# Performance work log

Measured on AMD Instinct MI355X. Metric: run time of the kernel, lower is better.

Reference implementation:

```python
import jax, jax.numpy as jnp
import numpy as np

B, A, H = 128, 24, 256
N, E = B * A, B * A * A
MAX_ATOMS, TIME_DIM, TEXT_DIM, NFREQ, NLAYERS = 103, 256, 128, 10, 4
DIS_DIM = NFREQ * 2 * 3  # 60
EDGE_IN = 2 * H + 9 + DIS_DIM  # 581


def setup_inputs() -> dict:
    key = jax.random.key(0)
    ks = iter(jax.random.split(key, 40))
    def nrm(shape, fan_in):
        return jax.random.normal(next(ks), shape, jnp.float32) / np.sqrt(fan_in).astype(np.float32)
    # fully-connected block-diagonal edges per graph (incl. self-loops), as dense_to_sparse(block_diag(ones))
    ii = jnp.repeat(jnp.arange(A, dtype=jnp.int32), A)
    jj = jnp.tile(jnp.arange(A, dtype=jnp.int32), A)
    off = (jnp.arange(B, dtype=jnp.int32) * A)[:, None]
    edges = jnp.stack([(off + ii[None, :]).reshape(-1), (off + jj[None, :]).reshape(-1)])  # [2,E]
    node2graph = jnp.repeat(jnp.arange(B, dtype=jnp.int32), A)  # [N]
    edge2graph = node2graph[edges[0]]  # [E]
    return dict(
        atom_types=jax.random.normal(next(ks), (N, MAX_ATOMS), jnp.float32),
        frac_coords=jax.random.uniform(next(ks), (N, 3), jnp.float32),
        lattices=jax.random.normal(next(ks), (B, 3, 3), jnp.float32),
        t=jax.random.normal(next(ks), (B, TIME_DIM), jnp.float32),
        text_embeds=jax.random.normal(next(ks), (B, TEXT_DIM), jnp.float32),
        w_emb=nrm((H, MAX_ATOMS), MAX_ATOMS), b_emb=jnp.zeros((H,), jnp.float32),
        w_cond=nrm((2 * H, TIME_DIM + TEXT_DIM), TIME_DIM + TEXT_DIM), b_cond=jnp.zeros((2 * H,), jnp.float32),
        w_proj=nrm((H, H), H), b_proj=jnp.zeros((H,), jnp.float32),
        film_g=jnp.ones((H,), jnp.float32), film_b=jnp.zeros((H,), jnp.float32),
        edge_w1=nrm((NLAYERS, H, EDGE_IN), EDGE_IN), edge_b1=jnp.zeros((NLAYERS, H), jnp.float32),
        edge_w2=nrm((NLAYERS, H, H), H), edge_b2=jnp.zeros((NLAYERS, H), jnp.float32),
        node_w1=nrm((NLAYERS, H, 2 * H), 2 * H), node_b1=jnp.zeros((NLAYERS, H), jnp.float32),
        node_w2=nrm((NLAYERS, H, H), H), node_b2=jnp.zeros((NLAYERS, H), jnp.float32),
        w_coord=nrm((3, H), H), w_latt=nrm((9, H), H),
        w_type=nrm((MAX_ATOMS, H), H), b_type=jnp.zeros((MAX_ATOMS,), jnp.float32),
        edges=edges, node2graph=node2graph, edge2graph=edge2graph,
    )


def _layernorm(x, g, b):
    mu = jnp.mean(x, -1, keepdims=True)
    v = jnp.mean((x - mu) ** 2, -1, keepdims=True)
    return (x - mu) * jax.lax.rsqrt(v + 1e-5) * g + b


def reference(atom_types, frac_coords, lattices, t, text_embeds,
              w_emb, b_emb, w_cond, b_cond, w_proj, b_proj, film_g, film_b,
              edge_w1, edge_b1, edge_w2, edge_b2, node_w1, node_b1, node_w2, node_b2,
              w_coord, w_latt, w_type, b_type, edges, node2graph, edge2graph):
    silu = jax.nn.silu
    e0, e1 = edges[0], edges[1]
    # gen_edges (fc): periodic fractional difference per edge
    frac_diff = (frac_coords[e1] - frac_coords[e0]) % 1.0  # [E,3]
    # SinusoidsEmbedding (detached in the original)
    freqs = 2.0 * jnp.pi * jnp.arange(NFREQ, dtype=jnp.float32)
    emb = (frac_diff[..., None] * freqs).reshape(frac_diff.shape[0], 3 * NFREQ)
    demb = jax.lax.stop_gradient(jnp.concatenate([jnp.sin(emb), jnp.cos(emb)], -1))  # [E,60]
    # lattice inner products (ip=True), gathered per edge
    lat_ips = jnp.einsum('bij,bkj->bik', lattices, lattices).reshape(-1, 9)
    lat_e = lat_ips[edge2graph]  # [E,9]
    # FiLM conditioning (identical every layer) -- repeat_interleave per atom == gather by node2graph
    cond = silu(jnp.concatenate([t, text_embeds], -1) @ w_cond.T + b_cond)[node2graph]  # [N,2H]
    scale, shift = cond[:, :H], cond[:, H:]
    deg = jnp.maximum(jax.ops.segment_sum(jnp.ones((e0.shape[0],), jnp.float32), e0, num_segments=N), 1.0)
    nf = atom_types @ w_emb.T + b_emb  # smooth node embedding: Linear(max_atoms, H)
    for i in range(NLAYERS):
        # FiLM layer
        y = _layernorm(nf @ w_proj.T + b_proj, film_g, film_b)
        nf = nf + silu(y * scale + shift)
        # CSPLayer edge model: gather -> concat -> 2-layer MLP
        ein = jnp.concatenate([nf[e0], nf[e1], lat_e, demb], -1)  # [E, 581]
        ef = silu(ein @ edge_w1[i].T + edge_b1[i])
        ef = silu(ef @ edge_w2[i].T + edge_b2[i])
        # node model: scatter_mean over source nodes, then 2-layer MLP, residual
        agg = jax.ops.segment_sum(ef, e0, num_segments=N) / deg[:, None]
        no = silu(jnp.concatenate([nf, agg], -1) @ node_w1[i].T + node_b1[i])
        no = silu(no @ node_w2[i].T + node_b2[i])
        nf = nf + no
    coords_out = nf @ w_coord.T  # [N,3]
    gfeat = jax.ops.segment_sum(nf, node2graph, num_segments=B) / jnp.float32(A)  # scatter mean over graphs
    lattice_out = (gfeat @ w_latt.T).reshape(-1, 3, 3)
    lattice_out = jnp.einsum('bij,bjk->bik', lattice_out, lattices)  # ip=True
    atom_types_out = nf @ w_type.T + b_type  # [N,103]
    return atom_types_out, lattice_out, coords_out, nf
```

## Files before the change

### kernel.cpp

```cpp
#include <hip/hip_runtime.h>
#include <math.h>

#define B_      128
#define A_      24
#define N_      3072
#define NLAYERS 4

#define OFF_COND    0
#define OFF_LATW    65536
#define OFF_NFMIDH  196608
#define OFF_AGGH    589824
#define OFF_PARTIH  983040
#define OFF_PARTJH  1376256
#define OFF_W1LATT  1769472
#define OFF_PW1A    1778688
#define OFF_PW1B    1909760
#define OFF_PW1D    2040832
#define OFF_PW2     2073600
#define OFF_PWPROJ  2204672
#define OFF_PNW1    2237440
#define OFF_PNW2    2499584
#define OFF_PWEMB   2630656
#define OFF_PWCOND  2647040
#define OFF_PWTYPE  2745344

#define OUT_TYPES  0
#define OUT_LATT   316416
#define OUT_COORD  317568
#define OUT_NF     326784

typedef __attribute__((ext_vector_type(8))) short bf16x8;
typedef __attribute__((ext_vector_type(4))) float f32x4;

__device__ __forceinline__ float silu_f(float x) { return x / (1.0f + __expf(-x)); }
__device__ __forceinline__ unsigned short f2bf(float x) {
    unsigned int u = __float_as_uint(x);
    return (unsigned short)((u + 0x7FFFu + ((u >> 16) & 1u)) >> 16);
}
__device__ __forceinline__ float bf2f(unsigned short h) {
    return __uint_as_float(((unsigned int)h) << 16);
}

__global__ void k_prep(const float* w_emb, const float* w_cond, const float* w_proj,
                       const float* ew1, const float* ew2, const float* nw1, const float* nw2,
                       const float* w_type, float* ws) {
    int idx = blockIdx.x * blockDim.x + threadIdx.x;
    unsigned short* pu = (unsigned short*)ws;
    int i = idx;
    if (i < 9216)   { int l = i / 2304, r = (i % 2304) / 256, h = i % 256;
                      ws[OFF_W1LATT + i] = ew1[((size_t)l * 256 + h) * 581 + 512 + r]; return; }        i -= 9216;
    if (i < 262144) { int l = i >> 16, r = i & 65535, ks = r >> 13, r2 = r & 8191,
                      nt = r2 >> 9, r3 = r2 & 511, lane = r3 >> 3, j = r3 & 7;
                      int k = ks * 32 + (lane >> 4) * 8 + j, n = nt * 16 + (lane & 15);
                      pu[(size_t)OFF_PW1A * 2 + i] = f2bf(ew1[((size_t)l * 256 + n) * 581 + k]); return; } i -= 262144;
    if (i < 262144) { int l = i >> 16, r = i & 65535, ks = r >> 13, r2 = r & 8191,
                      nt = r2 >> 9, r3 = r2 & 511, lane = r3 >> 3, j = r3 & 7;
                      int k = ks * 32 + (lane >> 4) * 8 + j, n = nt * 16 + (lane & 15);
                      pu[(size_t)OFF_PW1B * 2 + i] = f2bf(ew1[((size_t)l * 256 + n) * 581 + 256 + k]); return; } i -= 262144;
    if (i < 65536)  { int l = i >> 14, r = i & 16383, ks = r >> 13, r2 = r & 8191,
                      nt = r2 >> 9, r3 = r2 & 511, lane = r3 >> 3, j = r3 & 7;
                      int kp = ks * 32 + (lane >> 4) * 8 + j, n = nt * 16 + (lane & 15);
                      float v = (kp < 60) ? ew1[((size_t)l * 256 + n) * 581 + 521 + kp] : 0.0f;
                      pu[(size_t)OFF_PW1D * 2 + i] = f2bf(v); return; }                                  i -= 65536;
    if (i < 262144) { int l = i >> 16, r = i & 65535, ks = r >> 13, r2 = r & 8191,
                      nt = r2 >> 9, r3 = r2 & 511, lane = r3 >> 3, j = r3 & 7;
                      int k = ks * 32 + (lane >> 4) * 8 + j, n = nt * 16 + (lane & 15);
                      pu[(size_t)OFF_PW2 * 2 + i] = f2bf(ew2[((size_t)l * 256 + n) * 256 + k]); return; } i -= 262144;
    if (i < 65536)  { int ks = i >> 13, r2 = i & 8191,
                      nt = r2 >> 9, r3 = r2 & 511, lane = r3 >> 3, j = r3 & 7;
                      int k = ks * 32 + (lane >> 4) * 8 + j, n = nt * 16 + (lane & 15);
                      pu[(size_t)OFF_PWPROJ * 2 + i] = f2bf(w_proj[(size_t)n * 256 + k]); return; }      i -= 65536;
    if (i < 524288) { int l = i >> 17, r = i & 131071, ks = r >> 13, r2 = r & 8191,
                      nt = r2 >> 9, r3 = r2 & 511, lane = r3 >> 3, j = r3 & 7;
                      int k = ks * 32 + (lane >> 4) * 8 + j, n = nt * 16 + (lane & 15);
                      pu[(size_t)OFF_PNW1 * 2 + i] = f2bf(nw1[((size_t)l * 256 + n) * 512 + k]); return; } i -= 524288;
    if (i < 262144) { int l = i >> 16, r = i & 65535, ks = r >> 13, r2 = r & 8191,
                      nt = r2 >> 9, r3 = r2 & 511, lane = r3 >> 3, j = r3 & 7;
                      int k = ks * 32 + (lane >> 4) * 8 + j, n = nt * 16 + (lane & 15);
                      pu[(size_t)OFF_PNW2 * 2 + i] = f2bf(nw2[((size_t)l * 256 + n) * 256 + k]); return; } i -= 262144;
    if (i < 32768)  { int ks = i >> 13, r2 = i & 8191,
                      nt = r2 >> 9, r3 = r2 & 511, lane = r3 >> 3, j = r3 & 7;
                      int k = ks * 32 + (lane >> 4) * 8 + j, n = nt * 16 + (lane & 15);
                      float v = (k < 103) ? w_emb[(size_t)n * 103 + k] : 0.0f;
                      pu[(size_t)OFF_PWEMB * 2 + i] = f2bf(v); return; }                                 i -= 32768;
    if (i < 196608) { int ks = i / 16384, r2 = i & 16383,
                      nt = r2 >> 9, r3 = r2 & 511, lane = r3 >> 3, j = r3 & 7;
                      int k = ks * 32 + (lane >> 4) * 8 + j, n = nt * 16 + (lane & 15);
                      pu[(size_t)OFF_PWCOND * 2 + i] = f2bf(w_cond[(size_t)n * 384 + k]); return; }      i -= 196608;
    { int ks = i / 3584, r2 = i % 3584,
      nt = r2 >> 9, r3 = r2 & 511, lane = r3 >> 3, j = r3 & 7;
      int k = ks * 32 + (lane >> 4) * 8 + j, a = nt * 16 + (lane & 15);
      float v = (a < 103) ? w_type[(size_t)a * 256 + k] : 0.0f;
      pu[(size_t)OFF_PWTYPE * 2 + i] = f2bf(v); }
}

__global__ void __launch_bounds__(256) k_setup(const float* lat, const float* t_in, const float* tx,
                                               const float* b_cond, float* ws) {
    __shared__ __align__(16) unsigned short s_ct[16][392];
    __shared__ float s_lat[16][9];
    int tid = threadIdx.x, w = tid >> 6, ln = tid & 63;
    int l15 = ln & 15, g = ln >> 4;
    int g0 = blockIdx.x * 16;
    if (tid < 144) {
        int gl = tid / 9, r = tid % 9, ii = r / 3, kk = r % 3;
        const float* L = lat + (g0 + gl) * 9;
        s_lat[gl][r] = L[ii*3+0]*L[kk*3+0] + L[ii*3+1]*L[kk*3+1] + L[ii*3+2]*L[kk*3+2];
    }
    for (int idx = tid; idx < 16 * 384; idx += 256) {
        int row = idx / 384, k = idx % 384;
        float v = (k < 256) ? t_in[(size_t)(g0 + row) * 256 + k] : tx[(size_t)(g0 + row) * 128 + (k - 256)];
        s_ct[row][k] = f2bf(v);
    }
    __syncthreads();
    for (int idx = tid; idx < 16384; idx += 256) {
        int l = idx >> 12, gl = (idx >> 8) & 15, h = idx & 255;
        float a = 0.f;
#pragma unroll
        for (int r = 0; r < 9; r++) a += s_lat[gl][r] * ws[OFF_W1LATT + (l * 9 + r) * 256 + h];
        ws[OFF_LATW + (size_t)(l * 128 + g0 + gl) * 256 + h] = a;
    }
    const unsigned short* pc = (const unsigned short*)ws + (size_t)OFF_PWCOND * 2;
    f32x4 acc[8] = {};
    for (int ks = 0; ks < 12; ks++) {
        bf16x8 a = *(const bf16x8*)&s_ct[l15][ks * 32 + g * 8];
#pragma unroll
        for (int q = 0; q < 8; q++) {
            int nt = w * 8 + q;
            bf16x8 bf = *(const bf16x8*)&pc[((size_t)(ks * 32 + nt) * 64 + ln) * 8];
            acc[q] = __builtin_amdgcn_mfma_f32_16x16x32_bf16(a, bf, acc[q], 0, 0, 0);
        }
    }
#pragma unroll
    for (int q = 0; q < 8; q++) {
        int col = w * 128 + q * 16 + l15;
        float bc = b_cond[col];
#pragma unroll
        for (int r = 0; r < 4; r++) {
            int gg = g0 + 4 * g + r;
            ws[OFF_COND + (size_t)gg * 512 + col] = silu_f(acc[q][r] + bc);
        }
    }
}

__global__ void __launch_bounds__(512) k_fnf(int l, const float* at, const float* b_emb,
                                             const float* nb1, const float* nb2,
                                             const float* b_proj, const float* film_g, const float* film_b,
                                             const float* eb1, float* ws) {
    __shared__ __align__(16) unsigned short s_in[16][536];
    __shared__ __align__(16) unsigned short s_h[16][264];
    __shared__ __align__(16) unsigned short s_a[16][264];
    __shared__ float s_nf[16][260];
    __shared__ float s_mu[16], s_rs[16];
    float (*s_c)[268] = (float(*)[268])&s_in[0][0];
    int tid = threadIdx.x, w = tid >> 6, ln = tid & 63;
    int l15 = ln & 15, g = ln >> 4;
    int n0 = blockIdx.x * 16;
    const unsigned short* wsu = (const unsigned short*)ws;
    unsigned short* wsw = (unsigned short*)ws;

    f32x4 accn[2] = {};
    if (l == 0) {
        for (int idx = tid; idx < 16 * 128; idx += 512) {
            int row = idx >> 7, k = idx & 127;
            s_in[row][k] = (k < 103) ? f2bf(at[(size_t)(n0 + row) * 103 + k]) : (unsigned short)0;
        }
        __syncthreads();
        const unsigned short* pe = wsu + (size_t)OFF_PWEMB * 2;
        for (int ks = 0; ks < 4; ks++) {
            bf16x8 a = *(const bf16x8*)&s_in[l15][ks * 32 + g * 8];
#pragma unroll
            for (int q = 0; q < 2; q++) {
                bf16x8 bf = *(const bf16x8*)&pe[((size_t)(ks * 16 + 2 * w + q) * 64 + ln) * 8];
                accn[q] = __builtin_amdgcn_mfma_f32_16x16x32_bf16(a, bf, accn[q], 0, 0, 0);
            }
        }
        __syncthreads();
#pragma unroll
        for (int q = 0; q < 2; q++) {
            int col = w * 32 + q * 16 + l15;
            float be = b_emb[col];
#pragma unroll
            for (int r = 0; r < 4; r++) {
                int row = 4 * g + r;
                float v = accn[q][r] + be;
                s_nf[row][col] = v;
                s_a[row][col] = f2bf(v);
            }
        }
    } else {
        int lp = l - 1;
        const unsigned short* nfmidh = wsu + (size_t)OFF_NFMIDH * 2;
        const unsigned short* aggh   = wsu + (size_t)OFF_AGGH * 2;
        {
            int row = tid >> 5, c8 = tid & 31;
            *(uint4*)&s_in[row][c8 * 8]       = *(const uint4*)&nfmidh[(size_t)(n0 + row) * 256 + c8 * 8];
            *(uint4*)&s_in[row][256 + c8 * 8] = *(const uint4*)&aggh[(size_t)(n0 + row) * 256 + c8 * 8];
        }
        __syncthreads();
        const unsigned short* p1 = wsu + (size_t)OFF_PNW1 * 2 + (size_t)lp * 131072;
        f32x4 acc[2] = {};
        for (int ks = 0; ks < 16; ks++) {
            bf16x8 a = *(const bf16x8*)&s_in[l15][ks * 32 + g * 8];
#pragma unroll
            for (int q = 0; q < 2; q++) {
                bf16x8 bf = *(const bf16x8*)&p1[((size_t)(ks * 16 + 2 * w + q) * 64 + ln) * 8];
                acc[q] = __builtin_amdgcn_mfma_f32_16x16x32_bf16(a, bf, acc[q], 0, 0, 0);
            }
        }
#pragma unroll
        for (int q = 0; q < 2; q++) {
            int col = w * 32 + q * 16 + l15;
            float b1 = nb1[lp * 256 + col];
#pragma unroll
            for (int r = 0; r < 4; r++) s_h[4 * g + r][col] = f2bf(silu_f(acc[q][r] + b1));
        }
        __syncthreads();
        const unsigned short* p2 = wsu + (size_t)OFF_PNW2 * 2 + (size_t)lp * 65536;
        for (int ks = 0; ks < 8; ks++) {
            bf16x8 a = *(const bf16x8*)&s_h[l15][ks * 32 + g * 8];
#pragma unroll
            for (int q = 0; q < 2; q++) {
                bf16x8 bf = *(const bf16x8*)&p2[((size_t)(ks * 16 + 2 * w + q) * 64 + ln) * 8];
                accn[q] = __builtin_amdgcn_mfma_f32_16x16x32_bf16(a, bf, accn[q], 0, 0, 0);
            }
        }
#pragma unroll
        for (int q = 0; q < 2; q++) {
            int col = w * 32 + q * 16 + l15;
            float b2 = nb2[lp * 256 + col];
#pragma unroll
            for (int r = 0; r < 4; r++) {
                int row = 4 * g + r;
                float v = bf2f(s_in[row][col]) + silu_f(accn[q][r] + b2);
                s_nf[row][col] = v;
                s_a[row][col] = f2bf(v);
            }
        }
    }
    __syncthreads();
    const unsigned short* pwp = wsu + (size_t)OFF_PWPROJ * 2;
    f32x4 accp[2] = {};
    for (int ks = 0; ks < 8; ks++) {
        bf16x8 a = *(const bf16x8*)&s_a[l15][ks * 32 + g * 8];
#pragma unroll
        for (int q = 0; q < 2; q++) {
            bf16x8 bf = *(const bf16x8*)&pwp[((size_t)(ks * 16 + 2 * w + q) * 64 + ln) * 8];
            accp[q] = __builtin_amdgcn_mfma_f32_16x16x32_bf16(a, bf, accp[q], 0, 0, 0);
        }
    }
    __syncthreads();
#pragma unroll
    for (int q = 0; q < 2; q++) {
        int col = w * 32 + q * 16 + l15;
        float bp = b_proj[col];
#pragma unroll
        for (int r = 0; r < 4; r++) s_c[4 * g + r][col] = accp[q][r] + bp;
    }
    __syncthreads();
    for (int r2 = 0; r2 < 2; r2++) {
        int row = w * 2 + r2;
        float s = 0.f, q = 0.f;
        for (int c = ln; c < 256; c += 64) { float v = s_c[row][c]; s += v; q += v * v; }
#pragma unroll
        for (int o = 1; o < 64; o <<= 1) { s += __shfl_xor(s, o); q += __shfl_xor(q, o); }
        if (ln == 0) {
            float mu = s * (1.0f / 256.0f);
            float var = q * (1.0f / 256.0f) - mu * mu;
            s_mu[row] = mu; s_rs[row] = rsqrtf(var + 1e-5f);
        }
    }
    __syncthreads();
    {
        int col = tid & 255, rb = tid >> 8;
        float gg = film_g[col], bb = film_b[col];
        unsigned short* nfmidh = wsw + (size_t)OFF_NFMIDH * 2;
#pragma unroll
        for (int t = 0; t < 8; t++) {
            int row = rb + 2 * t;
            int n = n0 + row, b = n / 24;
            float sc = ws[OFF_COND + (size_t)b * 512 + col];
            float sh = ws[OFF_COND + (size_t)b * 512 + 256 + col];
            float yn = (s_c[row][col] - s_mu[row]) * s_rs[row] * gg + bb;
            float outv = s_nf[row][col] + silu_f(yn * sc + sh);
            unsigned short ob = f2bf(outv);
            nfmidh[(size_t)n * 256 + col] = ob;
            s_a[row][col] = ob;
        }
    }
    __syncthreads();
    const unsigned short* pA = wsu + (size_t)OFF_PW1A * 2 + (size_t)l * 65536;
    const unsigned short* pB = wsu + (size_t)OFF_PW1B * 2 + (size_t)l * 65536;
    f32x4 aI[2] = {}, aJ[2] = {};
    for (int ks = 0; ks < 8; ks++) {
        bf16x8 a = *(const bf16x8*)&s_a[l15][ks * 32 + g * 8];
#pragma unroll
        for (int q = 0; q < 2; q++) {
            bf16x8 bi = *(const bf16x8*)&pA[((size_t)(ks * 16 + 2 * w + q) * 64 + ln) * 8];
            bf16x8 bj = *(const bf16x8*)&pB[((size_t)(ks * 16 + 2 * w + q) * 64 + ln) * 8];
            aI[q] = __builtin_amdgcn_mfma_f32_16x16x32_bf16(a, bi, aI[q], 0, 0, 0);
            aJ[q] = __builtin_amdgcn_mfma_f32_16x16x32_bf16(a, bj, aJ[q], 0, 0, 0);
        }
    }
    unsigned short* partih = wsw + (size_t)OFF_PARTIH * 2;
    unsigned short* partjh = wsw + (size_t)OFF_PARTJH * 2;
#pragma unroll
    for (int q = 0; q < 2; q++) {
        int col = w * 32 + q * 16 + l15;
        float e1 = eb1[l * 256 + col];
#pragma unroll
        for (int r = 0; r < 4; r++) {
            int n = n0 + 4 * g + r;
            int gb = n / 24;
            float vi = aI[q][r] + e1 + ws[OFF_LATW + (size_t)(l * 128 + gb) * 256 + col];
            partih[(size_t)n * 256 + col] = f2bf(vi);
            partjh[(size_t)n * 256 + col] = f2bf(aJ[q][r]);
        }
    }
}

__global__ void __launch_bounds__(256, 4) k_edge(int l, const float* frac, const float* eb2, float* ws) {
    __shared__ __align__(16) unsigned short s_u[48 * 256];
    __shared__ __align__(16) unsigned short s_pJ[24][264];
    __shared__ __align__(16) unsigned short s_pI[2][264];
    __shared__ float s_fc[24][3];
    int tid = threadIdx.x, w = tid >> 6, ln = tid & 63;
    int l15 = ln & 15, g = ln >> 4;
    int b = blockIdx.x & 127, c = blockIdx.x >> 7;
    int i0 = c * 2;

    const unsigned short* partjh = (const unsigned short*)ws + (size_t)OFF_PARTJH * 2 + (size_t)b * 24 * 256;
    const unsigned short* partih = (const unsigned short*)ws + (size_t)OFF_PARTIH * 2 + (size_t)(b * 24 + i0) * 256;
    for (int idx = tid; idx < 72; idx += 256) s_fc[idx / 3][idx % 3] = frac[b * 72 + idx];
    for (int idx = tid; idx < 768; idx += 256) {
        int row = idx >> 5, c8 = idx & 31;
        *(uint4*)&s_pJ[row][c8 * 8] = *(const uint4*)&partjh[row * 256 + c8 * 8];
    }
    if (tid < 64) {
        int row = tid >> 5, c8 = tid & 31;
        *(uint4*)&s_pI[row][c8 * 8] = *(const uint4*)&partih[row * 256 + c8 * 8];
    }
    __syncthreads();
    for (int idx = tid; idx < 3072; idx += 256) {
        int row = idx >> 6, k = idx & 63;
        unsigned short v = 0;
        if (k < 60) {
            int kk = (k < 30) ? k : k - 30;
            int d = kk / 10, f = kk % 10;
            int hi = (row >= 24);
            int j = row - (hi ? 24 : 0);
            float fd = s_fc[j][d] - s_fc[i0 + hi][d];
            fd -= floorf(fd);
            float ang = fd * (6.283185307179586f * (float)f);
            v = f2bf((k < 30) ? __sinf(ang) : __cosf(ang));
        }
        s_u[(row << 6) + (((k >> 3) ^ (row & 7)) << 3) + (k & 7)] = v;
    }
    __syncthreads();

    const unsigned short* wsu = (const unsigned short*)ws;
    const unsigned short* pw1d = wsu + (size_t)OFF_PW1D * 2 + (size_t)l * 16384;
    f32x4 acc[3][4] = {};
    for (int ks = 0; ks < 2; ks++) {
        bf16x8 a[3];
        int kb = ks * 4 + g;
#pragma unroll
        for (int mt = 0; mt < 3; mt++) {
            int row = mt * 16 + l15;
            a[mt] = *(const bf16x8*)&s_u[(row << 6) + ((kb ^ (row & 7)) << 3)];
        }
#pragma unroll
        for (int nt = 0; nt < 4; nt++) {
            bf16x8 bf = *(const bf16x8*)&pw1d[((size_t)(ks * 16 + w * 4 + nt) * 64 + ln) * 8];
#pragma unroll
            for (int mt = 0; mt < 3; mt++)
                acc[mt][nt] = __builtin_amdgcn_mfma_f32_16x16x32_bf16(a[mt], bf, acc[mt][nt], 0, 0, 0);
        }
    }
    __syncthreads();
    float pIv[2][4];
#pragma unroll
    for (int hi = 0; hi < 2; hi++)
#pragma unroll
        for (int nt = 0; nt < 4; nt++) pIv[hi][nt] = bf2f(s_pI[hi][w * 64 + nt * 16 + l15]);
#pragma unroll
    for (int mt = 0; mt < 3; mt++)
#pragma unroll
        for (int nt = 0; nt < 4; nt++) {
            int col = w * 64 + nt * 16 + l15;
#pragma unroll
            for (int r = 0; r < 4; r++) {
                int row = mt * 16 + 4 * g + r;
                int hi = (row >= 24);
                int j = row - 24 * hi;
                float v = acc[mt][nt][r] + pIv[hi][nt] + bf2f(s_pJ[j][col]);
                s_u[(row << 8) + ((((col >> 3) ^ (row & 7))) << 3) + (col & 7)] = f2bf(silu_f(v));
            }
        }
    __syncthreads();
    const unsigned short* pw2 = wsu + (size_t)OFF_PW2 * 2 + (size_t)l * 65536;
    f32x4 acc2[3][4] = {};
    for (int ks = 0; ks < 8; ks++) {
        bf16x8 a[3];
        int kb = ks * 4 + g;
#pragma unroll
        for (int mt = 0; mt < 3; mt++) {
            int row = mt * 16 + l15;
            a[mt] = *(const bf16x8*)&s_u[(row << 8) + ((kb ^ (row & 7)) << 3)];
        }
#pragma unroll
        for (int nt = 0; nt < 4; nt++) {
            bf16x8 bf = *(const bf16x8*)&pw2[((size_t)(ks * 16 + w * 4 + nt) * 64 + ln) * 8];
#pragma unroll
            for (int mt = 0; mt < 3; mt++)
                acc2[mt][nt] = __builtin_amdgcn_mfma_f32_16x16x32_bf16(a[mt], bf, acc2[mt][nt], 0, 0, 0);
        }
    }
    float s0[4] = {}, s1[4] = {};
#pragma unroll
    for (int nt = 0; nt < 4; nt++) {
        int col = w * 64 + nt * 16 + l15;
        float b2 = eb2[l * 256 + col];
#pragma unroll
        for (int r = 0; r < 4; r++) s0[nt] += silu_f(acc2[0][nt][r] + b2);
        float m = 0.f;
#pragma unroll
        for (int r = 0; r < 4; r++) m += silu_f(acc2[1][nt][r] + b2);
        if (g < 2) s0[nt] += m; else s1[nt] += m;
#pragma unroll
        for (int r = 0; r < 4; r++) s1[nt] += silu_f(acc2[2][nt][r] + b2);
    }
#pragma unroll
    for (int nt = 0; nt < 4; nt++) {
        s0[nt] += __shfl_xor(s0[nt], 16);
        s0[nt] += __shfl_xor(s0[nt], 32);
        s1[nt] += __shfl_xor(s1[nt], 16);
        s1[nt] += __shfl_xor(s1[nt], 32);
    }
    unsigned short* aggh = (unsigned short*)ws + (size_t)OFF_AGGH * 2;
    if (g == 0) {
#pragma unroll
        for (int nt = 0; nt < 4; nt++) {
            int col = w * 64 + nt * 16 + l15;
            aggh[(size_t)(b * 24 + i0) * 256 + col]     = f2bf(s0[nt] * (1.0f / 24.0f));
            aggh[(size_t)(b * 24 + i0 + 1) * 256 + col] = f2bf(s1[nt] * (1.0f / 24.0f));
        }
    }
}

__global__ void __launch_bounds__(512) k_tail(const float* nb1, const float* nb2,
                                              const float* b_type, const float* w_coord,
                                              const float* lattices, const float* w_latt,
                                              float* ws, float* out) {
    __shared__ __align__(16) unsigned short s_in[32][536];
    __shared__ __align__(16) unsigned short s_h[32][264];
    __shared__ float gf[256];
    __shared__ float lo[9];
    float (*s_nf)[260] = (float(*)[260])&s_in[0][0];
    unsigned short (*s_a)[264] = s_h;
    int tid = threadIdx.x, w = tid >> 6, ln = tid & 63;
    int l15 = ln & 15, g = ln >> 4;
    int b = blockIdx.x, n0 = b * 24;
    const unsigned short* wsu = (const unsigned short*)ws;
    const int lp = 3;
    const unsigned short* nfmidh = wsu + (size_t)OFF_NFMIDH * 2;
    const unsigned short* aggh   = wsu + (size_t)OFF_AGGH * 2;
    for (int idx = tid; idx < 1024; idx += 512) {
        int row = idx >> 5, c8 = idx & 31;
        int rr = (row < 24) ? row : 0;
        *(uint4*)&s_in[row][c8 * 8]       = *(const uint4*)&nfmidh[(size_t)(n0 + rr) * 256 + c8 * 8];
        *(uint4*)&s_in[row][256 + c8 * 8] = *(const uint4*)&aggh[(size_t)(n0 + rr) * 256 + c8 * 8];
    }
    __syncthreads();
    const unsigned short* p1 = wsu + (size_t)OFF_PNW1 * 2 + (size_t)lp * 131072;
    f32x4 acc[2][2] = {};
    for (int ks = 0; ks < 16; ks++) {
        bf16x8 a0 = *(const bf16x8*)&s_in[l15][ks * 32 + g * 8];
        bf16x8 a1 = *(const bf16x8*)&s_in[16 + l15][ks * 32 + g * 8];
#pragma unroll
        for (int q = 0; q < 2; q++) {
            bf16x8 bf = *(const bf16x8*)&p1[((size_t)(ks * 16 + 2 * w + q) * 64 + ln) * 8];
            acc[0][q] = __builtin_amdgcn_mfma_f32_16x16x32_bf16(a0, bf, acc[0][q], 0, 0, 0);
            acc[1][q] = __builtin_amdgcn_mfma_f32_16x16x32_bf16(a1, bf, acc[1][q], 0, 0, 0);
        }
    }
#pragma unroll
    for (int q = 0; q < 2; q++) {
        int col = w * 32 + q * 16 + l15;
        float b1 = nb1[lp * 256 + col];
#pragma unroll
        for (int mt = 0; mt < 2; mt++)
#pragma unroll
            for (int r = 0; r < 4; r++) s_h[mt * 16 + 4 * g + r][col] = f2bf(silu_f(acc[mt][q][r] + b1));
    }
    __syncthreads();
    const unsigned short* p2 = wsu + (size_t)OFF_PNW2 * 2 + (size_t)lp * 65536;
    f32x4 a2[2][2] = {};
    for (int ks = 0; ks < 8; ks++) {
        bf16x8 a0 = *(const bf16x8*)&s_h[l15][ks * 32 + g * 8];
        bf16x8 a1 = *(const bf16x8*)&s_h[16 + l15][ks * 32 + g * 8];
#pragma unroll
        for (int q = 0; q < 2; q++) {
            bf16x8 bf = *(const bf16x8*)&p2[((size_t)(ks * 16 + 2 * w + q) * 64 + ln) * 8];
            a2[0][q] = __builtin_amdgcn_mfma_f32_16x16x32_bf16(a0, bf, a2[0][q], 0, 0, 0);
            a2[1][q] = __builtin_amdgcn_mfma_f32_16x16x32_bf16(a1, bf, a2[1][q], 0, 0, 0);
        }
    }
    float res[2][2][4];
#pragma unroll
    for (int q = 0; q < 2; q++) {
        int col = w * 32 + q * 16 + l15;
#pragma unroll
        for (int mt = 0; mt < 2; mt++)
#pragma unroll
            for (int r = 0; r < 4; r++) res[mt][q][r] = bf2f(s_in[mt * 16 + 4 * g + r][col]);
    }
    __syncthreads();
#pragma unroll
    for (int q = 0; q < 2; q++) {
        int col = w * 32 + q * 16 + l15;
        float b2 = nb2[lp * 256 + col];
#pragma unroll
        for (int mt = 0; mt < 2; mt++)
#pragma unroll
            for (int r = 0; r < 4; r++) {
                int row = mt * 16 + 4 * g + r;
                float v = res[mt][q][r] + silu_f(a2[mt][q][r] + b2);
                if (row < 24) {
                    s_nf[row][col] = v;
                    out[OUT_NF + (size_t)(n0 + row) * 256 + col] = v;
                }
                s_a[row][col] = f2bf(v);
            }
    }
    __syncthreads();
    if (w < 7) {
        const unsigned short* pt = wsu + (size_t)OFF_PWTYPE * 2;
        f32x4 at2[2] = {};
        for (int ks = 0; ks < 8; ks++) {
            bf16x8 a0 = *(const bf16x8*)&s_a[l15][ks * 32 + g * 8];
            bf16x8 a1 = *(const bf16x8*)&s_a[16 + l15][ks * 32 + g * 8];
            bf16x8 bf = *(const bf16x8*)&pt[((size_t)(ks * 7 + w) * 64 + ln) * 8];
            at2[0] = __builtin_amdgcn_mfma_f32_16x16x32_bf16(a0, bf, at2[0], 0, 0, 0);
            at2[1] = __builtin_amdgcn_mfma_f32_16x16x32_bf16(a1, bf, at2[1], 0, 0, 0);
        }
        int a_col = w * 16 + l15;
        if (a_col < 103) {
            float bt = b_type[a_col];
#pragma unroll
            for (int mt = 0; mt < 2; mt++)
#pragma unroll
                for (int r = 0; r < 4; r++) {
                    int row = mt * 16 + 4 * g + r;
                    if (row < 24)
                        out[OUT_TYPES + (size_t)(n0 + row) * 103 + a_col] = at2[mt][r] + bt;
                }
        }
    }
    if (tid < 72) {
        int p = tid / 3, cc = tid % 3;
        float a0 = 0.f;
        for (int k = 0; k < 256; k++) a0 += s_nf[p][k] * w_coord[cc * 256 + k];
        out[OUT_COORD + (size_t)(n0 + p) * 3 + cc] = a0;
    }
    if (tid < 256) {
        float s = 0.f;
#pragma unroll
        for (int i = 0; i < 24; i++) s += s_nf[i][tid];
        gf[tid] = s * (1.0f / 24.0f);
    }
    __syncthreads();
    if (tid < 9) {
        float a0 = 0.f;
        for (int k = 0; k < 256; k++) a0 += gf[k] * w_latt[tid * 256 + k];
        lo[tid] = a0;
    }
    __syncthreads();
    if (tid < 9) {
        int i = tid / 3, kk = tid % 3;
        float a0 = 0.f;
#pragma unroll
        for (int j = 0; j < 3; j++) a0 += lo[i * 3 + j] * lattices[b * 9 + j * 3 + kk];
        out[OUT_LATT + (size_t)b * 9 + tid] = a0;
    }
}

extern "C" void kernel_launch(void* const* d_in, const int* in_sizes, int n_in,
                              void* d_out, int out_size, void* d_ws, size_t ws_size,
                              hipStream_t stream) {
    const float* atom_types = (const float*)d_in[0];
    const float* frac       = (const float*)d_in[1];
    const float* lattices   = (const float*)d_in[2];
    const float* t_in       = (const float*)d_in[3];
    const float* text       = (const float*)d_in[4];
    const float* w_emb      = (const float*)d_in[5];
    const float* b_emb      = (const float*)d_in[6];
    const float* w_cond     = (const float*)d_in[7];
    const float* b_cond     = (const float*)d_in[8];
    const float* w_proj     = (const float*)d_in[9];
    const float* b_proj     = (const float*)d_in[10];
    const float* film_g     = (const float*)d_in[11];
    const float* film_b     = (const float*)d_in[12];
    const float* ew1        = (const float*)d_in[13];
    const float* eb1        = (const float*)d_in[14];
    const float* ew2        = (const float*)d_in[15];
    const float* eb2        = (const float*)d_in[16];
    const float* nw1        = (const float*)d_in[17];
    const float* nb1        = (const float*)d_in[18];
    const float* nw2        = (const float*)d_in[19];
    const float* nb2        = (const float*)d_in[20];
    const float* w_coord    = (const float*)d_in[21];
    const float* w_latt     = (const float*)d_in[22];
    const float* w_type     = (const float*)d_in[23];
    const float* b_type     = (const float*)d_in[24];
    float* ws  = (float*)d_ws;
    float* out = (float*)d_out;

    k_prep<<<7700, 256, 0, stream>>>(w_emb, w_cond, w_proj, ew1, ew2, nw1, nw2, w_type, ws);
    k_setup<<<8, 256, 0, stream>>>(lattices, t_in, text, b_cond, ws);
    for (int l = 0; l < NLAYERS; l++) {
        k_fnf<<<N_ / 16, 512, 0, stream>>>(l, atom_types, b_emb, nb1, nb2,
                                           b_proj, film_g, film_b, eb1, ws);
        k_edge<<<N_ * 12 / 24, 256, 0, stream>>>(l, frac, eb2, ws);
    }
    k_tail<<<B_, 512, 0, stream>>>(nb1, nb2, b_type, w_coord, lattices, w_latt, ws, out);
}
```

Measured before the change: 348.8 us.

## Precompute distance embeddings once and fold node partials into edge MFMA via one-hot

The sinusoidal distance embedding for every edge tile is now computed once in the prep kernel and stored in bf16 in the workspace. Each edge layer loads it instead of recomputing sin/cos. The per-node I and J partial sums are also added through an extra MFMA K-step, using one-hot selector columns in the A tile and the partial rows as the B operand, which removes the shared-memory staging and per-element adds in the epilogue. The cost is a much larger prep launch that writes about 9 MB of embeddings, global reads of that buffer in each of the 4 layers, and one extra MFMA step per tile. The one-hot path also adds the partials in bf16 precision inside the MFMA.

```diff
diff --git a/kernel.cpp b/kernel.cpp
--- a/kernel.cpp
+++ b/kernel.cpp
@@ -23,6 +23,7 @@
 #define OFF_PWEMB   2630656
 #define OFF_PWCOND  2647040
 #define OFF_PWTYPE  2745344
+#define OFF_DEMBG   2759680
 
 #define OUT_TYPES  0
 #define OUT_LATT   316416
@@ -43,7 +44,7 @@
 
 __global__ void k_prep(const float* w_emb, const float* w_cond, const float* w_proj,
                        const float* ew1, const float* ew2, const float* nw1, const float* nw2,
-                       const float* w_type, float* ws) {
+                       const float* w_type, const float* frac, float* ws) {
     int idx = blockIdx.x * blockDim.x + threadIdx.x;
     unsigned short* pu = (unsigned short*)ws;
     int i = idx;
@@ -87,11 +88,27 @@
                       nt = r2 >> 9, r3 = r2 & 511, lane = r3 >> 3, j = r3 & 7;
                       int k = ks * 32 + (lane >> 4) * 8 + j, n = nt * 16 + (lane & 15);
                       pu[(size_t)OFF_PWCOND * 2 + i] = f2bf(w_cond[(size_t)n * 384 + k]); return; }      i -= 196608;
-    { int ks = i / 3584, r2 = i % 3584,
-      nt = r2 >> 9, r3 = r2 & 511, lane = r3 >> 3, j = r3 & 7;
-      int k = ks * 32 + (lane >> 4) * 8 + j, a = nt * 16 + (lane & 15);
-      float v = (a < 103) ? w_type[(size_t)a * 256 + k] : 0.0f;
-      pu[(size_t)OFF_PWTYPE * 2 + i] = f2bf(v); }
+    if (i < 28672)  { int ks = i / 3584, r2 = i % 3584,
+                      nt = r2 >> 9, r3 = r2 & 511, lane = r3 >> 3, j = r3 & 7;
+                      int k = ks * 32 + (lane >> 4) * 8 + j, a = nt * 16 + (lane & 15);
+                      float v = (a < 103) ? w_type[(size_t)a * 256 + k] : 0.0f;
+                      pu[(size_t)OFF_PWTYPE * 2 + i] = f2bf(v); return; }                                i -= 28672;
+    if (i < 4718592) {
+        int u = i / 3072, r2 = i % 3072, row = r2 >> 6, k = r2 & 63;
+        int bb = u / 12, c = u % 12, i0 = 2 * c;
+        unsigned short v = 0;
+        if (k < 60) {
+            int kk = (k < 30) ? k : k - 30;
+            int d = kk / 10, f = kk % 10;
+            int hi = (row >= 24);
+            int j = row - 24 * hi;
+            float fd = frac[(bb * 24 + j) * 3 + d] - frac[(bb * 24 + i0 + hi) * 3 + d];
+            fd -= floorf(fd);
+            float ang = fd * (6.283185307179586f * (float)f);
+            v = f2bf((k < 30) ? __sinf(ang) : __cosf(ang));
+        }
+        pu[(size_t)OFF_DEMBG * 2 + i] = v;
+    }
 }
 
 __global__ void __launch_bounds__(256) k_setup(const float* lat, const float* t_in, const float* tx,
@@ -318,70 +335,68 @@
     }
 }
 
-__global__ void __launch_bounds__(256, 4) k_edge(int l, const float* frac, const float* eb2, float* ws) {
+__global__ void __launch_bounds__(256, 4) k_edge(int l, const float* eb2, float* ws) {
     __shared__ __align__(16) unsigned short s_u[48 * 256];
-    __shared__ __align__(16) unsigned short s_pJ[24][264];
-    __shared__ __align__(16) unsigned short s_pI[2][264];
-    __shared__ float s_fc[24][3];
     int tid = threadIdx.x, w = tid >> 6, ln = tid & 63;
     int l15 = ln & 15, g = ln >> 4;
     int b = blockIdx.x & 127, c = blockIdx.x >> 7;
-    int i0 = c * 2;
-
-    const unsigned short* partjh = (const unsigned short*)ws + (size_t)OFF_PARTJH * 2 + (size_t)b * 24 * 256;
-    const unsigned short* partih = (const unsigned short*)ws + (size_t)OFF_PARTIH * 2 + (size_t)(b * 24 + i0) * 256;
-    for (int idx = tid; idx < 72; idx += 256) s_fc[idx / 3][idx % 3] = frac[b * 72 + idx];
-    for (int idx = tid; idx < 768; idx += 256) {
-        int row = idx >> 5, c8 = idx & 31;
-        *(uint4*)&s_pJ[row][c8 * 8] = *(const uint4*)&partjh[row * 256 + c8 * 8];
-    }
-    if (tid < 64) {
-        int row = tid >> 5, c8 = tid & 31;
-        *(uint4*)&s_pI[row][c8 * 8] = *(const uint4*)&partih[row * 256 + c8 * 8];
-    }
-    __syncthreads();
-    for (int idx = tid; idx < 3072; idx += 256) {
-        int row = idx >> 6, k = idx & 63;
-        unsigned short v = 0;
-        if (k < 60) {
-            int kk = (k < 30) ? k : k - 30;
-            int d = kk / 10, f = kk % 10;
-            int hi = (row >= 24);
-            int j = row - (hi ? 24 : 0);
-            float fd = s_fc[j][d] - s_fc[i0 + hi][d];
-            fd -= floorf(fd);
-            float ang = fd * (6.283185307179586f * (float)f);
-            v = f2bf((k < 30) ? __sinf(ang) : __cosf(ang));
-        }
-        s_u[(row << 6) + (((k >> 3) ^ (row & 7)) << 3) + (k & 7)] = v;
-    }
-    __syncthreads();
-
+    int i0 = c * 2, n0i = b * 24;
     const unsigned short* wsu = (const unsigned short*)ws;
+
+    const unsigned short* partih = wsu + (size_t)OFF_PARTIH * 2;
+    const unsigned short* partjh = wsu + (size_t)OFF_PARTJH * 2;
+    bf16x8 bp[4];
+#pragma unroll
+    for (int nt = 0; nt < 4; nt++) {
+        int col = w * 64 + nt * 16 + l15;
+#pragma unroll
+        for (int e = 0; e < 8; e++) {
+            int kp = g * 8 + e;
+            unsigned short v = 0;
+            if (kp < 2)       v = partih[(size_t)(n0i + i0 + kp) * 256 + col];
+            else if (kp < 26) v = partjh[(size_t)(n0i + kp - 2) * 256 + col];
+            bp[nt][e] = (short)v;
+        }
+    }
+    const unsigned short* dg = wsu + (size_t)OFF_DEMBG * 2 + (size_t)(b * 12 + c) * 3072;
+    for (int idx = tid; idx < 384; idx += 256) {
+        int row = idx >> 3, ch = idx & 7;
+        uint4 v = *(const uint4*)&dg[row * 64 + ch * 8];
+        *(uint4*)&s_u[row * 128 + ((ch ^ (row & 7)) << 3)] = v;
+    }
+    for (int idx = tid; idx < 384; idx += 256) {
+        int row = idx >> 3, ch = 8 + (idx & 7);
+        int hi = (row >= 24), j = row - 24 * hi;
+        unsigned short vals[8] = {0, 0, 0, 0, 0, 0, 0, 0};
+        int k0 = ch * 8 - 64;
+        if (hi >= k0 && hi < k0 + 8) vals[hi - k0] = 0x3F80;
+        int kj = 2 + j;
+        if (kj >= k0 && kj < k0 + 8) vals[kj - k0] = 0x3F80;
+        *(uint4*)&s_u[row * 128 + ((ch ^ (row & 7)) << 3)] = *(uint4*)vals;
+    }
+    __syncthreads();
+
     const unsigned short* pw1d = wsu + (size_t)OFF_PW1D * 2 + (size_t)l * 16384;
     f32x4 acc[3][4] = {};
-    for (int ks = 0; ks < 2; ks++) {
+#pragma unroll
+    for (int ks = 0; ks < 3; ks++) {
         bf16x8 a[3];
         int kb = ks * 4 + g;
 #pragma unroll
         for (int mt = 0; mt < 3; mt++) {
             int row = mt * 16 + l15;
-            a[mt] = *(const bf16x8*)&s_u[(row << 6) + ((kb ^ (row & 7)) << 3)];
+            a[mt] = *(const bf16x8*)&s_u[row * 128 + ((kb ^ (row & 7)) << 3)];
         }
 #pragma unroll
         for (int nt = 0; nt < 4; nt++) {
-            bf16x8 bf = *(const bf16x8*)&pw1d[((size_t)(ks * 16 + w * 4 + nt) * 64 + ln) * 8];
+            bf16x8 bf = (ks < 2) ? *(const bf16x8*)&pw1d[((size_t)(ks * 16 + w * 4 + nt) * 64 + ln) * 8]
+                                 : bp[nt];
 #pragma unroll
             for (int mt = 0; mt < 3; mt++)
                 acc[mt][nt] = __builtin_amdgcn_mfma_f32_16x16x32_bf16(a[mt], bf, acc[mt][nt], 0, 0, 0);
         }
     }
     __syncthreads();
-    float pIv[2][4];
-#pragma unroll
-    for (int hi = 0; hi < 2; hi++)
-#pragma unroll
-        for (int nt = 0; nt < 4; nt++) pIv[hi][nt] = bf2f(s_pI[hi][w * 64 + nt * 16 + l15]);
 #pragma unroll
     for (int mt = 0; mt < 3; mt++)
 #pragma unroll
@@ -390,10 +405,7 @@
 #pragma unroll
             for (int r = 0; r < 4; r++) {
                 int row = mt * 16 + 4 * g + r;
-                int hi = (row >= 24);
-                int j = row - 24 * hi;
-                float v = acc[mt][nt][r] + pIv[hi][nt] + bf2f(s_pJ[j][col]);
-                s_u[(row << 8) + ((((col >> 3) ^ (row & 7))) << 3) + (col & 7)] = f2bf(silu_f(v));
+                s_u[(row << 8) + ((((col >> 3) ^ (row & 7))) << 3) + (col & 7)] = f2bf(silu_f(acc[mt][nt][r]));
             }
         }
     __syncthreads();
@@ -441,8 +453,8 @@
 #pragma unroll
         for (int nt = 0; nt < 4; nt++) {
             int col = w * 64 + nt * 16 + l15;
-            aggh[(size_t)(b * 24 + i0) * 256 + col]     = f2bf(s0[nt] * (1.0f / 24.0f));
-            aggh[(size_t)(b * 24 + i0 + 1) * 256 + col] = f2bf(s1[nt] * (1.0f / 24.0f));
+            aggh[(size_t)(n0i + i0) * 256 + col]     = f2bf(s0[nt] * (1.0f / 24.0f));
+            aggh[(size_t)(n0i + i0 + 1) * 256 + col] = f2bf(s1[nt] * (1.0f / 24.0f));
         }
     }
 }
@@ -615,12 +627,12 @@
     float* ws  = (float*)d_ws;
     float* out = (float*)d_out;
 
-    k_prep<<<7700, 256, 0, stream>>>(w_emb, w_cond, w_proj, ew1, ew2, nw1, nw2, w_type, ws);
+    k_prep<<<26132, 256, 0, stream>>>(w_emb, w_cond, w_proj, ew1, ew2, nw1, nw2, w_type, frac, ws);
     k_setup<<<8, 256, 0, stream>>>(lattices, t_in, text, b_cond, ws);
     for (int l = 0; l < NLAYERS; l++) {
         k_fnf<<<N_ / 16, 512, 0, stream>>>(l, atom_types, b_emb, nb1, nb2,
                                            b_proj, film_g, film_b, eb1, ws);
-        k_edge<<<N_ * 12 / 24, 256, 0, stream>>>(l, frac, eb2, ws);
+        k_edge<<<N_ * 12 / 24, 256, 0, stream>>>(l, eb2, ws);
     }
     k_tail<<<B_, 512, 0, stream>>>(nb1, nb2, b_type, w_coord, lattices, w_latt, ws, out);
 }
```

After: 356.8 us. 1.02x slower.
